# Optimization experiments

Measured on AMD Instinct MI355X. Metric: run time of the kernel, lower is better.

## Reference

```python
import jax, jax.numpy as jnp
import numpy as np

B, LMAX, NCOND, NHID = 256, 512, 300, 600

def setup_inputs() -> dict:
    key = jax.random.key(0)
    ks = jax.random.split(key, 7)
    x = jax.random.normal(ks[0], (B, NCOND), dtype=jnp.float32)
    context = jax.random.normal(ks[1], (B, LMAX, NCOND), dtype=jnp.float32)
    lengths = jax.random.randint(ks[2], (B,), 0, LMAX, dtype=jnp.int32)
    W1 = jax.random.normal(ks[3], (NCOND, NHID), dtype=jnp.float32) * (1.0 / np.sqrt(NCOND))
    b1 = jax.random.normal(ks[4], (NHID,), dtype=jnp.float32) * 0.02
    Wa = jax.random.normal(ks[5], (NHID, NCOND), dtype=jnp.float32) * (1.0 / np.sqrt(NHID))
    ba = jax.random.normal(ks[6], (NCOND,), dtype=jnp.float32) * 0.02
    return {"x": x, "context": context, "lengths": lengths, "W1": W1, "b1": b1, "Wa": Wa, "ba": ba}

def reference(x, context, lengths, W1, b1, Wa, ba):
    # lengths clamped to >=1 (a ragged context is always non-empty)
    lens = jnp.maximum(lengths, 1)
    # valid-position mask over padded context: [B, L, 1]
    valid = (jnp.arange(LMAX)[None, :] < lens[:, None])[..., None].astype(context.dtype)
    # per-token MLP: relu(ctx @ W1 + b1)  -> [B, L, nhid]
    h = jax.nn.relu(jnp.einsum('blc,ch->blh', context, W1) + b1)
    # masked mean over valid tokens (ragged mean-pool) -> [B, nhid]
    pooled = jnp.sum(h * valid, axis=1) / lens[:, None].astype(context.dtype)
    # sigmoid gate -> [B, ncond], applied to x embeddings
    gate = jax.nn.sigmoid(jnp.einsum('bh,hc->bc', pooled, Wa) + ba)
    return gate * x
```

## Files before the change

kernel.cpp:

```cpp
#include <hip/hip_runtime.h>
#include <math.h>

#define BB     256
#define LMAX   512
#define NCOND  300
#define NHID   600
#define NSEG   8
#define CHUNK  64
#define KPAD   320
#define KLDS   328
#define NCOLP  640
#define NKC    10

typedef short s16x8 __attribute__((ext_vector_type(8)));
typedef float f32x4 __attribute__((ext_vector_type(4)));

__device__ inline unsigned short f2bf(float f) {
    unsigned int x = __float_as_uint(f);
    x += 0x7fffu + ((x >> 16) & 1u);
    return (unsigned short)(x >> 16);
}

__global__ __launch_bounds__(256) void k0_w1t(const float* __restrict__ W1,
                                              unsigned short* __restrict__ w1t)
{
    const int t     = blockIdx.x * 256 + threadIdx.x;
    const int lane  = t & 63;
    const int g     = t >> 6;
    const int ntile = g / NKC;
    const int kc    = g - ntile * NKC;
    const int n     = ntile * 16 + (lane & 15);
    const int kbase = kc * 32 + (lane >> 4) * 8;
    union { unsigned short us[8]; s16x8 v8; } u;
#pragma unroll
    for (int j = 0; j < 8; ++j) {
        const int k = kbase + j;
        const float w = (n < NHID && k < NCOND) ? W1[(size_t)k * NHID + n] : 0.f;
        u.us[j] = f2bf(w);
    }
    *(s16x8*)(w1t + (size_t)t * 8) = u.v8;
}

__global__ __launch_bounds__(256, 3) void k1_mfma_pool(
    const float* __restrict__ ctx, const int* __restrict__ lengths,
    const unsigned short* __restrict__ w1t, const float* __restrict__ b1,
    float* __restrict__ partial)
{
    const int b  = blockIdx.x;
    const int s  = blockIdx.y;
    const int ch = blockIdx.z;

    int count = lengths[b]; if (count < 1) count = 1;
    const int l0 = s * CHUNK;
    if (l0 >= count) return;
    const int valid = min(count - l0, CHUNK);

    const int tid  = threadIdx.x;
    const int lane = tid & 63;
    const int wv   = tid >> 6;
    const int ln15 = lane & 15;
    const int kg   = lane >> 4;

    __shared__ __align__(16) unsigned short atile[CHUNK * KLDS];

#pragma unroll
    for (int p = 0; p < 10; ++p) {
        const int i  = p * 256 + tid;
        const int r  = i / 40;
        const int c8 = i - r * 40;
        union { unsigned short us[8]; s16x8 v8; } u;
        if (r < valid && c8 < 38) {
            const float* src = ctx + ((size_t)b * LMAX + l0 + r) * NCOND + c8 * 8;
            const float4 v0 = *(const float4*)src;
            float4 v1 = make_float4(0.f, 0.f, 0.f, 0.f);
            if (c8 < 37) v1 = *(const float4*)(src + 4);
            u.us[0] = f2bf(v0.x); u.us[1] = f2bf(v0.y);
            u.us[2] = f2bf(v0.z); u.us[3] = f2bf(v0.w);
            u.us[4] = f2bf(v1.x); u.us[5] = f2bf(v1.y);
            u.us[6] = f2bf(v1.z); u.us[7] = f2bf(v1.w);
        } else {
#pragma unroll
            for (int j = 0; j < 8; ++j) u.us[j] = 0;
        }
        *(s16x8*)(atile + r * KLDS + c8 * 8) = u.v8;
    }
    __syncthreads();

    const int ntile0 = ch * 20 + wv * 5;
    const unsigned short* bbase = w1t + ((size_t)ntile0 * NKC * 64 + lane) * 8;
    const unsigned short* arow  = atile + ln15 * KLDS + kg * 8;

    f32x4 acc[5][4];
#pragma unroll
    for (int nt = 0; nt < 5; ++nt)
#pragma unroll
        for (int mt = 0; mt < 4; ++mt) acc[nt][mt] = (f32x4){0.f, 0.f, 0.f, 0.f};

    s16x8 bf[2][5];
#pragma unroll
    for (int nt = 0; nt < 5; ++nt) bf[0][nt] = *(const s16x8*)(bbase + nt * 5120);

#pragma unroll
    for (int kc = 0; kc < NKC; ++kc) {
        const int cur = kc & 1, nxt = cur ^ 1;
        if (kc < NKC - 1) {
#pragma unroll
            for (int nt = 0; nt < 5; ++nt)
                bf[nxt][nt] = *(const s16x8*)(bbase + nt * 5120 + (kc + 1) * 512);
        }
        s16x8 af[4];
#pragma unroll
        for (int mt = 0; mt < 4; ++mt)
            af[mt] = *(const s16x8*)(arow + mt * 16 * KLDS + kc * 32);
#pragma unroll
        for (int nt = 0; nt < 5; ++nt)
#pragma unroll
            for (int mt = 0; mt < 4; ++mt)
                acc[nt][mt] = __builtin_amdgcn_mfma_f32_16x16x32_bf16(
                    af[mt], bf[cur][nt], acc[nt][mt], 0, 0, 0);
    }

#pragma unroll
    for (int nt = 0; nt < 5; ++nt) {
        const int colg = ch * 320 + wv * 80 + nt * 16 + ln15;
        const float b1c = (colg < NHID) ? b1[colg] : 0.f;
        float ssum = 0.f;
#pragma unroll
        for (int mt = 0; mt < 4; ++mt) {
            const int rbase = mt * 16 + kg * 4;
#pragma unroll
            for (int r = 0; r < 4; ++r) {
                const float h = fmaxf(acc[nt][mt][r] + b1c, 0.f);
                if (rbase + r < valid) ssum += h;
            }
        }
        ssum += __shfl_xor(ssum, 16, 64);
        ssum += __shfl_xor(ssum, 32, 64);
        if (kg == 0 && colg < NHID)
            partial[((size_t)s * BB + b) * NHID + colg] = ssum;
    }
}

__global__ __launch_bounds__(640) void k2_gate(
    const float* __restrict__ x, const int* __restrict__ lengths,
    const float* __restrict__ partial, const float* __restrict__ Wa,
    const float* __restrict__ ba, float* __restrict__ out)
{
    const int b0  = blockIdx.x * 2;
    const int tid = threadIdx.x;

    __shared__ float pl[2][NHID];

    if (tid < NHID) {
#pragma unroll
        for (int bb = 0; bb < 2; ++bb) {
            int count = lengths[b0 + bb]; if (count < 1) count = 1;
            const int nch = (count + CHUNK - 1) >> 6;
            float ssum = 0.f;
            for (int sp = 0; sp < nch; ++sp)
                ssum += partial[((size_t)sp * BB + (b0 + bb)) * NHID + tid];
            pl[bb][tid] = ssum / (float)count;
        }
    }
    __syncthreads();

    if (tid < 2 * NCOND) {
        const int bb = tid / NCOND;
        const int n  = tid - bb * NCOND;
        const int b  = b0 + bb;
        float a0 = ba[n], a1 = 0.f, a2 = 0.f, a3 = 0.f;
        const float4* p4 = (const float4*)pl[bb];
        for (int h4 = 0; h4 < 148; h4 += 4) {
            const float4 pv0 = p4[h4];
            const float4 pv1 = p4[h4 + 1];
            const float4 pv2 = p4[h4 + 2];
            const float4 pv3 = p4[h4 + 3];
            const int hb = h4 * 4;
            a0 = fmaf(pv0.x, Wa[(size_t)(hb +  0) * NCOND + n], a0);
            a0 = fmaf(pv0.y, Wa[(size_t)(hb +  1) * NCOND + n], a0);
            a0 = fmaf(pv0.z, Wa[(size_t)(hb +  2) * NCOND + n], a0);
            a0 = fmaf(pv0.w, Wa[(size_t)(hb +  3) * NCOND + n], a0);
            a1 = fmaf(pv1.x, Wa[(size_t)(hb +  4) * NCOND + n], a1);
            a1 = fmaf(pv1.y, Wa[(size_t)(hb +  5) * NCOND + n], a1);
            a1 = fmaf(pv1.z, Wa[(size_t)(hb +  6) * NCOND + n], a1);
            a1 = fmaf(pv1.w, Wa[(size_t)(hb +  7) * NCOND + n], a1);
            a2 = fmaf(pv2.x, Wa[(size_t)(hb +  8) * NCOND + n], a2);
            a2 = fmaf(pv2.y, Wa[(size_t)(hb +  9) * NCOND + n], a2);
            a2 = fmaf(pv2.z, Wa[(size_t)(hb + 10) * NCOND + n], a2);
            a2 = fmaf(pv2.w, Wa[(size_t)(hb + 11) * NCOND + n], a2);
            a3 = fmaf(pv3.x, Wa[(size_t)(hb + 12) * NCOND + n], a3);
            a3 = fmaf(pv3.y, Wa[(size_t)(hb + 13) * NCOND + n], a3);
            a3 = fmaf(pv3.z, Wa[(size_t)(hb + 14) * NCOND + n], a3);
            a3 = fmaf(pv3.w, Wa[(size_t)(hb + 15) * NCOND + n], a3);
        }
        {
            const float4 pv0 = p4[148];
            const float4 pv1 = p4[149];
            a0 = fmaf(pv0.x, Wa[(size_t)592 * NCOND + n], a0);
            a0 = fmaf(pv0.y, Wa[(size_t)593 * NCOND + n], a0);
            a0 = fmaf(pv0.z, Wa[(size_t)594 * NCOND + n], a0);
            a0 = fmaf(pv0.w, Wa[(size_t)595 * NCOND + n], a0);
            a1 = fmaf(pv1.x, Wa[(size_t)596 * NCOND + n], a1);
            a1 = fmaf(pv1.y, Wa[(size_t)597 * NCOND + n], a1);
            a1 = fmaf(pv1.z, Wa[(size_t)598 * NCOND + n], a1);
            a1 = fmaf(pv1.w, Wa[(size_t)599 * NCOND + n], a1);
        }
        const float acc  = (a0 + a1) + (a2 + a3);
        const float gate = 1.0f / (1.0f + expf(-acc));
        out[(size_t)b * NCOND + n] = gate * x[(size_t)b * NCOND + n];
    }
}

extern "C" void kernel_launch(void* const* d_in, const int* in_sizes, int n_in,
                              void* d_out, int out_size, void* d_ws, size_t ws_size,
                              hipStream_t stream)
{
    const float* x       = (const float*)d_in[0];
    const float* ctx     = (const float*)d_in[1];
    const int*   lengths = (const int*)  d_in[2];
    const float* W1      = (const float*)d_in[3];
    const float* b1      = (const float*)d_in[4];
    const float* Wa      = (const float*)d_in[5];
    const float* ba      = (const float*)d_in[6];
    float*       out     = (float*)d_out;

    unsigned short* w1t     = (unsigned short*)d_ws;
    float*          partial = (float*)((char*)d_ws + 409600);

    k0_w1t<<<100, 256, 0, stream>>>(W1, w1t);
    k1_mfma_pool<<<dim3(BB, NSEG, 2), 256, 0, stream>>>(ctx, lengths, w1t, b1, partial);
    k2_gate<<<BB / 2, 640, 0, stream>>>(x, lengths, partial, Wa, ba, out);
}
```

Before: 301.6 us.

## Pre-convert context to swizzled bf16 and DMA tiles directly into LDS

Adds a separate kernel that converts the valid context rows to bf16 once, in a padded and XOR-swizzled layout in workspace. The MFMA kernel then fills its shared-memory tile with global_load_lds direct copies instead of loading fp32, converting and storing per block. Under the old layout the two column-half blocks each converted the same rows, so the conversion was done twice. The cost is an extra kernel launch plus a write and re-read of the bf16 buffer (about 84MB of workspace). The new path only runs when the workspace is large enough, otherwise it falls back to the old kernel.

```diff
diff --git a/kernel.cpp b/kernel.cpp
--- a/kernel.cpp
+++ b/kernel.cpp
@@ -9,11 +9,14 @@
 #define CHUNK  64
 #define KPAD   320
 #define KLDS   328
-#define NCOLP  640
 #define NKC    10
+
+#define AS1 __attribute__((address_space(1)))
+#define AS3 __attribute__((address_space(3)))
 
 typedef short s16x8 __attribute__((ext_vector_type(8)));
 typedef float f32x4 __attribute__((ext_vector_type(4)));
+typedef unsigned short u16x4 __attribute__((ext_vector_type(4)));
 
 __device__ inline unsigned short f2bf(float f) {
     unsigned int x = __float_as_uint(f);
@@ -39,6 +42,126 @@
         u.us[j] = f2bf(w);
     }
     *(s16x8*)(w1t + (size_t)t * 8) = u.v8;
+}
+
+__global__ __launch_bounds__(256) void k0b_cvt(const float* __restrict__ ctx,
+                                               const int* __restrict__ lengths,
+                                               unsigned short* __restrict__ ctx16)
+{
+    const int b = blockIdx.x, s = blockIdx.y, tid = threadIdx.x;
+    int count = lengths[b]; if (count < 1) count = 1;
+    if (s * CHUNK >= count) return;
+
+    const size_t inbase  = ((size_t)b * LMAX + s * CHUNK) * NCOND;
+    const float* src = ctx + inbase;
+    char* dst = (char*)(ctx16 + ((size_t)b * LMAX + s * CHUNK) * KPAD);
+
+#pragma unroll
+    for (int i = 0; i < 20; ++i) {
+        const int c   = i * 256 + tid;
+        const int row = c / 80;
+        const int q   = c - row * 80;
+        float4 v = make_float4(0.f, 0.f, 0.f, 0.f);
+        if (q < 75)
+            v = *(const float4*)(src + (size_t)row * NCOND + q * 4);
+        union { unsigned short us[4]; u16x4 v4; } o;
+        o.us[0] = f2bf(v.x); o.us[1] = f2bf(v.y);
+        o.us[2] = f2bf(v.z); o.us[3] = f2bf(v.w);
+        const int off = (row * 640 + q * 8) ^ ((row & 7) << 4);
+        *(u16x4*)(dst + off) = o.v4;
+    }
+}
+
+__global__ __launch_bounds__(256, 3) void k1_mfma_dma(
+    const unsigned short* __restrict__ ctx16, const int* __restrict__ lengths,
+    const unsigned short* __restrict__ w1t, const float* __restrict__ b1,
+    float* __restrict__ partial)
+{
+    const int b  = blockIdx.x;
+    const int s  = blockIdx.y;
+    const int ch = blockIdx.z;
+
+    int count = lengths[b]; if (count < 1) count = 1;
+    const int l0 = s * CHUNK;
+    if (l0 >= count) return;
+    const int valid = min(count - l0, CHUNK);
+
+    const int tid  = threadIdx.x;
+    const int lane = tid & 63;
+    const int wv   = tid >> 6;
+    const int ln15 = lane & 15;
+    const int kg   = lane >> 4;
+
+    __shared__ __align__(16) unsigned short atile[CHUNK * KPAD];
+
+    const char* gsrc = (const char*)(ctx16 + ((size_t)b * LMAX + l0) * KPAD);
+    char* lbase = (char*)atile;
+#pragma unroll
+    for (int r = 0; r < 10; ++r) {
+        const int off = (r * 4 + wv) * 1024;
+        __builtin_amdgcn_global_load_lds(
+            (const AS1 void*)(gsrc + off + lane * 16),
+            (AS3 void*)(lbase + off),
+            16, 0, 0);
+    }
+
+    const int ntile0 = ch * 20 + wv * 5;
+    const unsigned short* bbase = w1t + ((size_t)ntile0 * NKC * 64 + lane) * 8;
+    s16x8 bf[2][5];
+#pragma unroll
+    for (int nt = 0; nt < 5; ++nt) bf[0][nt] = *(const s16x8*)(bbase + nt * 5120);
+
+    __syncthreads();
+
+    const int swz   = (ln15 & 7) << 4;
+    const int abase = ln15 * 640 + kg * 16;
+    const char* ab  = (const char*)atile;
+
+    f32x4 acc[5][4];
+#pragma unroll
+    for (int nt = 0; nt < 5; ++nt)
+#pragma unroll
+        for (int mt = 0; mt < 4; ++mt) acc[nt][mt] = (f32x4){0.f, 0.f, 0.f, 0.f};
+
+#pragma unroll
+    for (int kc = 0; kc < NKC; ++kc) {
+        const int cur = kc & 1, nxt = cur ^ 1;
+        if (kc < NKC - 1) {
+#pragma unroll
+            for (int nt = 0; nt < 5; ++nt)
+                bf[nxt][nt] = *(const s16x8*)(bbase + nt * 5120 + (kc + 1) * 512);
+        }
+        s16x8 af[4];
+#pragma unroll
+        for (int mt = 0; mt < 4; ++mt)
+            af[mt] = *(const s16x8*)(ab + ((abase + mt * 10240 + kc * 64) ^ swz));
+#pragma unroll
+        for (int nt = 0; nt < 5; ++nt)
+#pragma unroll
+            for (int mt = 0; mt < 4; ++mt)
+                acc[nt][mt] = __builtin_amdgcn_mfma_f32_16x16x32_bf16(
+                    af[mt], bf[cur][nt], acc[nt][mt], 0, 0, 0);
+    }
+
+#pragma unroll
+    for (int nt = 0; nt < 5; ++nt) {
+        const int colg = ch * 320 + wv * 80 + nt * 16 + ln15;
+        const float b1c = (colg < NHID) ? b1[colg] : 0.f;
+        float ssum = 0.f;
+#pragma unroll
+        for (int mt = 0; mt < 4; ++mt) {
+            const int rbase = mt * 16 + kg * 4;
+#pragma unroll
+            for (int r = 0; r < 4; ++r) {
+                const float h = fmaxf(acc[nt][mt][r] + b1c, 0.f);
+                if (rbase + r < valid) ssum += h;
+            }
+        }
+        ssum += __shfl_xor(ssum, 16, 64);
+        ssum += __shfl_xor(ssum, 32, 64);
+        if (kg == 0 && colg < NHID)
+            partial[((size_t)s * BB + b) * NHID + colg] = ssum;
+    }
 }
 
 __global__ __launch_bounds__(256, 3) void k1_mfma_pool(
@@ -224,10 +347,23 @@
     const float* ba      = (const float*)d_in[6];
     float*       out     = (float*)d_out;
 
+    const size_t W1T_B   = 409600;
+    const size_t PART_B  = 4915200;
+    const size_t CTX16_B = (size_t)BB * LMAX * KPAD * 2;
+    const size_t NEED    = W1T_B + PART_B + CTX16_B;
+
     unsigned short* w1t     = (unsigned short*)d_ws;
-    float*          partial = (float*)((char*)d_ws + 409600);
+    float*          partial = (float*)((char*)d_ws + W1T_B);
 
     k0_w1t<<<100, 256, 0, stream>>>(W1, w1t);
-    k1_mfma_pool<<<dim3(BB, NSEG, 2), 256, 0, stream>>>(ctx, lengths, w1t, b1, partial);
+
+    if (ws_size >= NEED) {
+        unsigned short* ctx16 = (unsigned short*)((char*)d_ws + W1T_B + PART_B);
+        k0b_cvt<<<dim3(BB, NSEG), 256, 0, stream>>>(ctx, lengths, ctx16);
+        k1_mfma_dma<<<dim3(BB, NSEG, 2), 256, 0, stream>>>(ctx16, lengths, w1t, b1, partial);
+    } else {
+        k1_mfma_pool<<<dim3(BB, NSEG, 2), 256, 0, stream>>>(ctx, lengths, w1t, b1, partial);
+    }
+
     k2_gate<<<BB / 2, 640, 0, stream>>>(x, lengths, partial, Wa, ba, out);
 }
```

Result: slower. 309.5 us (+2.6%).

## Fuse both column halves into one block and swizzle LDS A tile

Applied to the files above, without the earlier changes.

Merges the two column-half blocks into a single 512-thread block computing all 640 hidden columns, so each context chunk is read from global memory and converted to bf16 once instead of twice. The padded LDS layout is replaced by an XOR-swizzled unpadded layout to avoid bank conflicts. Rows beyond the valid length are now loaded unconditionally and masked only at pooling. Larger blocks and the aggressive launch bound may limit registers and occupancy.

```diff
diff --git a/kernel.cpp b/kernel.cpp
--- a/kernel.cpp
+++ b/kernel.cpp
@@ -8,12 +8,11 @@
 #define NSEG   8
 #define CHUNK  64
 #define KPAD   320
-#define KLDS   328
-#define NCOLP  640
 #define NKC    10
 
 typedef short s16x8 __attribute__((ext_vector_type(8)));
 typedef float f32x4 __attribute__((ext_vector_type(4)));
+typedef unsigned short u16x8 __attribute__((ext_vector_type(8)));
 
 __device__ inline unsigned short f2bf(float f) {
     unsigned int x = __float_as_uint(f);
@@ -41,14 +40,13 @@
     *(s16x8*)(w1t + (size_t)t * 8) = u.v8;
 }
 
-__global__ __launch_bounds__(256, 3) void k1_mfma_pool(
+__global__ __launch_bounds__(512, 8) void k1_fused(
     const float* __restrict__ ctx, const int* __restrict__ lengths,
     const unsigned short* __restrict__ w1t, const float* __restrict__ b1,
     float* __restrict__ partial)
 {
-    const int b  = blockIdx.x;
-    const int s  = blockIdx.y;
-    const int ch = blockIdx.z;
+    const int b = blockIdx.x;
+    const int s = blockIdx.y;
 
     int count = lengths[b]; if (count < 1) count = 1;
     const int l0 = s * CHUNK;
@@ -61,34 +59,33 @@
     const int ln15 = lane & 15;
     const int kg   = lane >> 4;
 
-    __shared__ __align__(16) unsigned short atile[CHUNK * KLDS];
-
-#pragma unroll
-    for (int p = 0; p < 10; ++p) {
-        const int i  = p * 256 + tid;
-        const int r  = i / 40;
-        const int c8 = i - r * 40;
-        union { unsigned short us[8]; s16x8 v8; } u;
-        if (r < valid && c8 < 38) {
-            const float* src = ctx + ((size_t)b * LMAX + l0 + r) * NCOND + c8 * 8;
-            const float4 v0 = *(const float4*)src;
-            float4 v1 = make_float4(0.f, 0.f, 0.f, 0.f);
-            if (c8 < 37) v1 = *(const float4*)(src + 4);
-            u.us[0] = f2bf(v0.x); u.us[1] = f2bf(v0.y);
-            u.us[2] = f2bf(v0.z); u.us[3] = f2bf(v0.w);
-            u.us[4] = f2bf(v1.x); u.us[5] = f2bf(v1.y);
-            u.us[6] = f2bf(v1.z); u.us[7] = f2bf(v1.w);
-        } else {
-#pragma unroll
-            for (int j = 0; j < 8; ++j) u.us[j] = 0;
-        }
-        *(s16x8*)(atile + r * KLDS + c8 * 8) = u.v8;
+    __shared__ __align__(16) unsigned short atile[CHUNK * KPAD];
+
+    char* lds = (char*)atile;
+#pragma unroll
+    for (int p = 0; p < 5; ++p) {
+        const int i   = p * 512 + tid;
+        const int row = i / 40;
+        const int c8  = i - row * 40;
+        const float* rsrc = ctx + ((size_t)b * LMAX + l0 + row) * NCOND + c8 * 8;
+        float4 v0 = make_float4(0.f, 0.f, 0.f, 0.f);
+        float4 v1 = make_float4(0.f, 0.f, 0.f, 0.f);
+        if (c8 < 38) v0 = *(const float4*)rsrc;
+        if (c8 < 37) v1 = *(const float4*)(rsrc + 4);
+        union { unsigned short us[8]; u16x8 v8; } o;
+        o.us[0] = f2bf(v0.x); o.us[1] = f2bf(v0.y);
+        o.us[2] = f2bf(v0.z); o.us[3] = f2bf(v0.w);
+        o.us[4] = f2bf(v1.x); o.us[5] = f2bf(v1.y);
+        o.us[6] = f2bf(v1.z); o.us[7] = f2bf(v1.w);
+        const int off = (row * 640 + c8 * 16) ^ ((row & 7) << 4);
+        *(u16x8*)(lds + off) = o.v8;
     }
     __syncthreads();
 
-    const int ntile0 = ch * 20 + wv * 5;
-    const unsigned short* bbase = w1t + ((size_t)ntile0 * NKC * 64 + lane) * 8;
-    const unsigned short* arow  = atile + ln15 * KLDS + kg * 8;
+    const unsigned short* bbase = w1t + ((size_t)(wv * 5) * NKC * 64 + lane) * 8;
+    const int swz   = (ln15 & 7) << 4;
+    const int abase = ln15 * 640 + kg * 16;
+    const char* ab  = (const char*)atile;
 
     f32x4 acc[5][4];
 #pragma unroll
@@ -111,7 +108,7 @@
         s16x8 af[4];
 #pragma unroll
         for (int mt = 0; mt < 4; ++mt)
-            af[mt] = *(const s16x8*)(arow + mt * 16 * KLDS + kc * 32);
+            af[mt] = *(const s16x8*)(ab + ((abase + mt * 10240 + kc * 64) ^ swz));
 #pragma unroll
         for (int nt = 0; nt < 5; ++nt)
 #pragma unroll
@@ -122,7 +119,7 @@
 
 #pragma unroll
     for (int nt = 0; nt < 5; ++nt) {
-        const int colg = ch * 320 + wv * 80 + nt * 16 + ln15;
+        const int colg = wv * 80 + nt * 16 + ln15;
         const float b1c = (colg < NHID) ? b1[colg] : 0.f;
         float ssum = 0.f;
 #pragma unroll
@@ -228,6 +225,6 @@
     float*          partial = (float*)((char*)d_ws + 409600);
 
     k0_w1t<<<100, 256, 0, stream>>>(W1, w1t);
-    k1_mfma_pool<<<dim3(BB, NSEG, 2), 256, 0, stream>>>(ctx, lengths, w1t, b1, partial);
+    k1_fused<<<dim3(BB, NSEG), 512, 0, stream>>>(ctx, lengths, w1t, b1, partial);
     k2_gate<<<BB / 2, 640, 0, stream>>>(x, lengths, partial, Wa, ba, out);
 }
```

After: 819.1 us. 2.72x slower.
